# Kernel optimization log

Measured on AMD Instinct MI355X. Metric: run time of the kernel, lower is better.

Reference implementation:

```python
import jax, jax.numpy as jnp
import numpy as np

B, S, DIM = 8, 2048, 2048
M, N, DCTX = 4, 64, 1024
H, DH = 8, 64
INNER = H * DH
EPS = 1e-5


def _layernorm(x, g, b):
    mu = jnp.mean(x, axis=-1, keepdims=True)
    var = jnp.mean(jnp.square(x - mu), axis=-1, keepdims=True)
    return (x - mu) * jax.lax.rsqrt(var + EPS) * g + b


def setup_inputs() -> dict:
    key = jax.random.key(0)
    ks = jax.random.split(key, 5)
    return {
        "x": jax.random.normal(ks[0], (B, S, DIM), jnp.float32),
        "context": jax.random.normal(ks[1], (B, M, N, DCTX), jnp.float32),
        "ln_g": jnp.ones((DIM,), jnp.float32),
        "ln_b": jnp.zeros((DIM,), jnp.float32),
        "lnc_g": jnp.ones((DCTX,), jnp.float32),
        "lnc_b": jnp.zeros((DCTX,), jnp.float32),
        "Wq": jax.random.normal(ks[2], (DIM, INNER), jnp.float32) * (DIM ** -0.5),
        "Wkv": jax.random.normal(ks[3], (DCTX, 2 * INNER), jnp.float32) * (DCTX ** -0.5),
        "Wout": jax.random.normal(ks[4], (INNER, DIM), jnp.float32) * (INNER ** -0.5),
        "top_k": 32,
    }


def reference(x, context, ln_g, ln_b, lnc_g, lnc_b, Wq, Wkv, Wout, top_k):
    b, s, _ = x.shape
    kv_len = context.shape[1] * context.shape[2]
    scale = DH ** -0.5

    xn = _layernorm(x, ln_g, ln_b)                                  # [b, s, dim]
    cn = _layernorm(context.reshape(b, kv_len, DCTX), lnc_g, lnc_b)  # [b, mn, dctx]

    q = (xn @ Wq).reshape(b, s, H, DH).transpose(0, 2, 1, 3)        # [b, h, s, dh]
    kv = cn @ Wkv                                                   # [b, mn, 2*inner]
    k, v = jnp.split(kv, 2, axis=-1)
    k = k.reshape(b, kv_len, H, DH).transpose(0, 2, 1, 3)           # [b, h, mn, dh]
    v = v.reshape(b, kv_len, H, DH).transpose(0, 2, 1, 3)

    sim = jnp.einsum('bhid,bhjd->bhij', q, k) * scale               # [b, h, s, mn]
    topk_vals, topk_idx = jax.lax.top_k(sim, top_k)                 # [b, h, s, k]
    # softmax over -inf-masked sim == softmax over the top-k values scattered back
    attn_k = jax.nn.softmax(topk_vals, axis=-1)
    bi = jnp.arange(b)[:, None, None, None]
    hi = jnp.arange(H)[None, :, None, None]
    ii = jnp.arange(s)[None, None, :, None]
    attn = jnp.zeros_like(sim).at[bi, hi, ii, topk_idx].set(attn_k)  # [b, h, s, mn]

    out = jnp.einsum('bhij,bhjd->bhid', attn, v)                    # [b, h, s, dh]
    out = out.transpose(0, 2, 1, 3).reshape(b, s, INNER)
    return out @ Wout                                               # [b, s, dim]
```

## Files before the change

### kernel.cpp

```cpp
#include <hip/hip_runtime.h>
#include <hip/hip_bf16.h>


typedef __attribute__((ext_vector_type(8))) short short8;
typedef __attribute__((ext_vector_type(8))) _Float16 half8;
typedef __attribute__((ext_vector_type(4))) float f32x4;
typedef unsigned int u32;
typedef unsigned short u16;
typedef unsigned long long u64;

#define DI __device__ __forceinline__
#define DELTA 1.5e-4f
#define BLEND_GAP 5e-5
#define FCAP 131072u

DI u16 f2bf(float f) {
  u32 u = __builtin_bit_cast(u32, f);
  u = (u + 0x7FFFu + ((u >> 16) & 1u)) >> 16;
  return (u16)u;
}
DI float bf2f(u16 h) { u32 u = ((u32)h) << 16; return __builtin_bit_cast(float, u); }
DI u16 f2h(float f) { _Float16 h = (_Float16)f; return __builtin_bit_cast(u16, h); }
DI float h2f(u16 b) { return (float)__builtin_bit_cast(_Float16, b); }

DI f32x4 mfma16(short8 a, short8 b, f32x4 c) {
  return __builtin_amdgcn_mfma_f32_16x16x32_bf16(a, b, c, 0, 0, 0);
}
DI f32x4 mfma16h(half8 a, half8 b, f32x4 c) {
  return __builtin_amdgcn_mfma_f32_16x16x32_f16(a, b, c, 0, 0, 0);
}

DI void gload_lds16(const u16* g, u16* l) {
  __builtin_amdgcn_global_load_lds(
      (const __attribute__((address_space(1))) void*)g,
      (__attribute__((address_space(3))) void*)l, 16, 0, 0);
}

__global__ void k_zero(u32* p) { if (threadIdx.x < 8) p[threadIdx.x] = 0; }

__global__ __launch_bounds__(1024) void k_transpose_split(
    const float* __restrict__ src, u16* __restrict__ dh, u16* __restrict__ dl,
    int R, int C, float scale) {
  __shared__ float tile[32][33];
  const int tx = threadIdx.x, ty = threadIdx.y;
  const int c0 = blockIdx.x * 32, r0 = blockIdx.y * 32;
  tile[ty][tx] = src[(size_t)(r0 + ty) * C + (c0 + tx)];
  __syncthreads();
  const float f = tile[tx][ty] * scale;
  const u16 h = f2bf(f);
  const size_t o = (size_t)(c0 + ty) * R + (r0 + tx);
  dh[o] = h;
  dl[o] = f2bf(f - bf2f(h));
}

__global__ __launch_bounds__(1024) void k_transpose_f16(
    const float* __restrict__ src, u16* __restrict__ dst, int R, int C) {
  __shared__ float tile[32][33];
  const int tx = threadIdx.x, ty = threadIdx.y;
  const int c0 = blockIdx.x * 32, r0 = blockIdx.y * 32;
  tile[ty][tx] = src[(size_t)(r0 + ty) * C + (c0 + tx)];
  __syncthreads();
  dst[(size_t)(c0 + ty) * R + (r0 + tx)] = f2h(tile[tx][ty]);
}

__global__ __launch_bounds__(1024) void k_transpose_f32(
    const float* __restrict__ src, float* __restrict__ dst, int R, int C) {
  __shared__ float tile[32][33];
  const int tx = threadIdx.x, ty = threadIdx.y;
  const int c0 = blockIdx.x * 32, r0 = blockIdx.y * 32;
  tile[ty][tx] = src[(size_t)(r0 + ty) * C + (c0 + tx)];
  __syncthreads();
  dst[(size_t)(c0 + ty) * R + (r0 + tx)] = tile[tx][ty];
}

template<int C>
__global__ __launch_bounds__(256) void k_layernorm_split(
    const float* __restrict__ x, const float* __restrict__ g, const float* __restrict__ bb,
    u16* __restrict__ oh, u16* __restrict__ ol) {
  constexpr int NV = C / 256;
  const int t = threadIdx.x;
  const size_t row = blockIdx.x;
  const float* xr = x + row * C + t * NV;
  float v[NV]; float s = 0.f, sq = 0.f;
#pragma unroll
  for (int j = 0; j < NV; j += 4) {
    const float4 f = *(const float4*)(xr + j);
    v[j] = f.x; v[j + 1] = f.y; v[j + 2] = f.z; v[j + 3] = f.w;
    s += (f.x + f.y) + (f.z + f.w);
    sq += (f.x * f.x + f.y * f.y) + (f.z * f.z + f.w * f.w);
  }
#pragma unroll
  for (int off = 32; off >= 1; off >>= 1) { s += __shfl_xor(s, off); sq += __shfl_xor(sq, off); }
  __shared__ float red[8];
  if ((t & 63) == 0) { red[t >> 6] = s; red[4 + (t >> 6)] = sq; }
  __syncthreads();
  s = (red[0] + red[1]) + (red[2] + red[3]);
  sq = (red[4] + red[5]) + (red[6] + red[7]);
  const float mu = s * (1.0f / C);
  const float rs = rsqrtf(sq * (1.0f / C) - mu * mu + 1e-5f);
  u16 hh[NV], ll[NV];
#pragma unroll
  for (int j = 0; j < NV; j += 4) {
    const float4 gg = *(const float4*)(g + t * NV + j);
    const float4 bv = *(const float4*)(bb + t * NV + j);
    float f0 = (v[j] - mu) * rs * gg.x + bv.x;
    float f1 = (v[j + 1] - mu) * rs * gg.y + bv.y;
    float f2 = (v[j + 2] - mu) * rs * gg.z + bv.z;
    float f3 = (v[j + 3] - mu) * rs * gg.w + bv.w;
    hh[j] = f2bf(f0); ll[j] = f2bf(f0 - bf2f(hh[j]));
    hh[j + 1] = f2bf(f1); ll[j + 1] = f2bf(f1 - bf2f(hh[j + 1]));
    hh[j + 2] = f2bf(f2); ll[j + 2] = f2bf(f2 - bf2f(hh[j + 2]));
    hh[j + 3] = f2bf(f3); ll[j + 3] = f2bf(f3 - bf2f(hh[j + 3]));
  }
  if constexpr (NV == 8) {
    *(uint4*)(oh + row * C + t * NV) = *(const uint4*)hh;
    *(uint4*)(ol + row * C + t * NV) = *(const uint4*)ll;
  } else {
    *(uint2*)(oh + row * C + t * NV) = *(const uint2*)hh;
    *(uint2*)(ol + row * C + t * NV) = *(const uint2*)ll;
  }
}

__global__ __launch_bounds__(256) void k_gemm_split(
    const u16* __restrict__ Ah, const u16* __restrict__ Al,
    const u16* __restrict__ Bh, const u16* __restrict__ Bl,
    u16* __restrict__ Oh, u16* __restrict__ Ol, u16* __restrict__ Op,
    int M, int N, int K, int splitc) {
  __shared__ __align__(1024) u16 sAh[4096], sAl[4096], sBh[4096], sBl[4096];
  const int t = threadIdx.x;
  const int w = t >> 6, l = t & 63, lg = l >> 4, lr = l & 15;
  const int nwg = gridDim.x;
  const int cpx = nwg >> 3;
  const int swz = (blockIdx.x & 7) * cpx + (blockIdx.x >> 3);
  const int nbx = N >> 7;
  const size_t row0 = (size_t)(swz / nbx) * 128;
  const size_t col0 = (size_t)(swz % nbx) * 128;
  const size_t wrow0 = row0 + (size_t)(w >> 1) * 64;
  const size_t wcol0 = col0 + (size_t)(w & 1) * 64;
  const int srow0 = w * 32 + (l >> 2);
  const int skk = (l & 3) * 8;
  f32x4 acc[4][4];
  const f32x4 z4 = {0.f, 0.f, 0.f, 0.f};
#pragma unroll
  for (int i = 0; i < 4; ++i)
#pragma unroll
    for (int j = 0; j < 4; ++j) acc[i][j] = z4;
  for (int k0 = 0; k0 < K; k0 += 32) {
#pragma unroll
    for (int iss = 0; iss < 2; ++iss) {
      const int sr = srow0 + iss * 16;
      const int ub = (w * 32 + iss * 16) * 32;
      const size_t ga = (row0 + sr) * (size_t)K + k0 + skk;
      const size_t gb = (col0 + sr) * (size_t)K + k0 + skk;
      gload_lds16(Ah + ga, sAh + ub);
      gload_lds16(Al + ga, sAl + ub);
      gload_lds16(Bh + gb, sBh + ub);
      gload_lds16(Bl + gb, sBl + ub);
    }
    __syncthreads();
    short8 ah[4], al[4], bh[4], bl[4];
#pragma unroll
    for (int mt = 0; mt < 4; ++mt) {
      const int r = (w >> 1) * 64 + mt * 16 + lr;
      ah[mt] = *(const short8*)(sAh + r * 32 + lg * 8);
      al[mt] = *(const short8*)(sAl + r * 32 + lg * 8);
    }
#pragma unroll
    for (int nt = 0; nt < 4; ++nt) {
      const int c = (w & 1) * 64 + nt * 16 + lr;
      bh[nt] = *(const short8*)(sBh + c * 32 + lg * 8);
      bl[nt] = *(const short8*)(sBl + c * 32 + lg * 8);
    }
#pragma unroll
    for (int mt = 0; mt < 4; ++mt)
#pragma unroll
      for (int nt = 0; nt < 4; ++nt) {
        f32x4 a = acc[mt][nt];
        a = mfma16(al[mt], bh[nt], a);
        a = mfma16(ah[mt], bl[nt], a);
        a = mfma16(ah[mt], bh[nt], a);
        acc[mt][nt] = a;
      }
    __syncthreads();
  }
#pragma unroll
  for (int mt = 0; mt < 4; ++mt)
#pragma unroll
    for (int nt = 0; nt < 4; ++nt)
#pragma unroll
      for (int i = 0; i < 4; ++i) {
        const size_t r = wrow0 + mt * 16 + lg * 4 + i;
        const size_t c = wcol0 + nt * 16 + lr;
        const float f = acc[mt][nt][i];
        if ((int)c < splitc) {
          const u16 h = f2bf(f);
          Oh[r * (size_t)splitc + c] = h;
          Ol[r * (size_t)splitc + c] = f2bf(f - bf2f(h));
        } else {
          Op[r * (size_t)(N - splitc) + (c - splitc)] = f2h(f);
        }
      }
}

__global__ __launch_bounds__(256) void k_gemm_f16_f32(
    const u16* __restrict__ A, const u16* __restrict__ Bt, float* __restrict__ C,
    int M, int N, int K) {
  __shared__ __align__(1024) u16 sA[4096], sB[4096];
  const int t = threadIdx.x;
  const int w = t >> 6, l = t & 63, lg = l >> 4, lr = l & 15;
  const int nwg = gridDim.x;
  const int cpx = nwg >> 3;
  const int swz = (blockIdx.x & 7) * cpx + (blockIdx.x >> 3);
  const int nbx = N >> 7;
  const size_t row0 = (size_t)(swz / nbx) * 128;
  const size_t col0 = (size_t)(swz % nbx) * 128;
  const size_t wrow0 = row0 + (size_t)(w >> 1) * 64;
  const size_t wcol0 = col0 + (size_t)(w & 1) * 64;
  const int srow0 = w * 32 + (l >> 2);
  const int skk = (l & 3) * 8;
  f32x4 acc[4][4];
  const f32x4 z4 = {0.f, 0.f, 0.f, 0.f};
#pragma unroll
  for (int i = 0; i < 4; ++i)
#pragma unroll
    for (int j = 0; j < 4; ++j) acc[i][j] = z4;
  for (int k0 = 0; k0 < K; k0 += 32) {
#pragma unroll
    for (int iss = 0; iss < 2; ++iss) {
      const int sr = srow0 + iss * 16;
      const int ub = (w * 32 + iss * 16) * 32;
      const size_t ga = (row0 + sr) * (size_t)K + k0 + skk;
      const size_t gb = (col0 + sr) * (size_t)K + k0 + skk;
      gload_lds16(A + ga, sA + ub);
      gload_lds16(Bt + gb, sB + ub);
    }
    __syncthreads();
    half8 a[4], b[4];
#pragma unroll
    for (int mt = 0; mt < 4; ++mt) {
      const int r = (w >> 1) * 64 + mt * 16 + lr;
      a[mt] = __builtin_bit_cast(half8, *(const short8*)(sA + r * 32 + lg * 8));
    }
#pragma unroll
    for (int nt = 0; nt < 4; ++nt) {
      const int c = (w & 1) * 64 + nt * 16 + lr;
      b[nt] = __builtin_bit_cast(half8, *(const short8*)(sB + c * 32 + lg * 8));
    }
#pragma unroll
    for (int mt = 0; mt < 4; ++mt)
#pragma unroll
      for (int nt = 0; nt < 4; ++nt) acc[mt][nt] = mfma16h(a[mt], b[nt], acc[mt][nt]);
    __syncthreads();
  }
#pragma unroll
  for (int mt = 0; mt < 4; ++mt)
#pragma unroll
    for (int nt = 0; nt < 4; ++nt)
#pragma unroll
      for (int i = 0; i < 4; ++i)
        C[(wrow0 + mt * 16 + lg * 4 + i) * (size_t)N + wcol0 + nt * 16 + lr] = acc[mt][nt][i];
}

__global__ __launch_bounds__(256) void k_attn(
    const u16* __restrict__ qh, const u16* __restrict__ ql,
    const u16* __restrict__ kh, const u16* __restrict__ kl,
    const u16* __restrict__ vv, u16* __restrict__ ao,
    u32* __restrict__ fcnt, u32* __restrict__ flist) {
  extern __shared__ unsigned char smem[];
  unsigned char* khmem = smem;
  unsigned char* vmem = smem + 32768;

  const int t = threadIdx.x;
  const int gid = blockIdx.x;
  const int sblk = gid & 31, hh = (gid >> 5) & 7, b = gid >> 8;
  const size_t base = ((size_t)b * 256) * 512 + hh * 64;

  {
    const int jb = t >> 3;
    const int d0 = (t & 7) * 8;
#pragma unroll
    for (int rep = 0; rep < 8; ++rep) {
      const int j = rep * 32 + jb;
      const int sw = (j & 7) << 4;
      const uint4 kh4 = *(const uint4*)(kh + base + (size_t)j * 512 + d0);
      *(uint4*)(khmem + ((j * 128 + d0 * 2) ^ sw)) = kh4;
      const uint4 v4 = *(const uint4*)(vv + base + (size_t)j * 512 + d0);
      const u16* ev = (const u16*)&v4;
#pragma unroll
      for (int i = 0; i < 8; ++i) {
        const int d = d0 + i;
        const int mix = ((d & 7) ^ (d >> 3)) & 7;
        *(u16*)(vmem + ((d * 512 + j * 2) ^ (mix << 4))) = ev[i];
      }
    }
  }
  __syncthreads();

  const int w = t >> 6, l = t & 63, lg = l >> 4, lr = l & 15;
  const int s0 = sblk * 64 + w * 16;
  const u16* qpb = qh + ((size_t)(b * 2048 + s0 + lr)) * 512 + hh * 64 + lg * 8;
  const u16* qpl = ql + ((size_t)(b * 2048 + s0 + lr)) * 512 + hh * 64 + lg * 8;
  const short8 qh0 = *(const short8*)(qpb);
  const short8 qh1 = *(const short8*)(qpb + 32);
  const short8 ql0 = *(const short8*)(qpl);
  const short8 ql1 = *(const short8*)(qpl + 32);

  f32x4 acc[16];
  const f32x4 z4 = {0.f, 0.f, 0.f, 0.f};
#pragma unroll
  for (int ct = 0; ct < 16; ++ct) {
    const int j = ct * 16 + lr;
    const int sw = (j & 7) << 4;
    const short8 kB0 = *(const short8*)(khmem + ((j * 128 + lg * 16) ^ sw));
    const short8 kB1 = *(const short8*)(khmem + ((j * 128 + 64 + lg * 16) ^ sw));
    const short8 kC0 = *(const short8*)(kl + base + (size_t)j * 512 + lg * 8);
    const short8 kC1 = *(const short8*)(kl + base + (size_t)j * 512 + 32 + lg * 8);
    f32x4 z = z4;
    z = mfma16(ql0, kC0, z); z = mfma16(ql1, kC1, z);
    z = mfma16(ql0, kB0, z); z = mfma16(ql1, kB1, z);
    z = mfma16(qh0, kC0, z); z = mfma16(qh1, kC1, z);
    z = mfma16(qh0, kB0, z); z = mfma16(qh1, kB1, z);
    acc[ct] = z;
  }
  __syncthreads();

  unsigned char* wmem = khmem + w * 8192;
#pragma unroll
  for (int r = 0; r < 4; ++r) {
    float v[16]; u32 o[16];
#pragma unroll
    for (int c2 = 0; c2 < 16; ++c2) {
      const float f = acc[c2][r];
      v[c2] = f;
      const u32 u = __builtin_bit_cast(u32, f);
      o[c2] = (u & 0x80000000u) ? ~u : (u | 0x80000000u);
    }
    u32 lo = 0;
    for (int bit = 31; bit >= 0; --bit) {
      const u32 mid = lo | (1u << bit);
      int c = 0;
#pragma unroll
      for (int c2 = 0; c2 < 16; ++c2) c += (o[c2] >= mid) ? 1 : 0;
      c += __shfl_xor(c, 1); c += __shfl_xor(c, 2); c += __shfl_xor(c, 4); c += __shfl_xor(c, 8);
      lo = (c >= 32) ? mid : lo;
    }
    const u32 thr = lo;
    int cgt = 0; u32 m16 = 0;
#pragma unroll
    for (int c2 = 0; c2 < 16; ++c2) {
      cgt += (o[c2] > thr) ? 1 : 0;
      m16 |= (o[c2] == thr) ? (1u << c2) : 0u;
    }
    cgt += __shfl_xor(cgt, 1); cgt += __shfl_xor(cgt, 2); cgt += __shfl_xor(cgt, 4); cgt += __shfl_xor(cgt, 8);
    const int need = 32 - cgt;
    u32 selm = 0; int pre = 0;
#pragma unroll
    for (int c2 = 0; c2 < 16; ++c2) {
      const u64 bal = __ballot((int)((m16 >> c2) & 1u));
      const u32 gb = (u32)((bal >> (lg * 16)) & 0xFFFFull);
      const int rank = pre + __popc(gb & ((1u << lr) - 1u));
      selm |= (((m16 >> c2) & 1u) && rank < need) ? (1u << c2) : 0u;
      pre += __popc(gb);
    }
    {
      const u32 tu = (thr & 0x80000000u) ? (thr & 0x7FFFFFFFu) : ~thr;
      const float t32f = __builtin_bit_cast(float, tu);
      float m33 = -3.0e38f;
#pragma unroll
      for (int c2 = 0; c2 < 16; ++c2) {
        const bool se = (o[c2] > thr) || ((selm >> c2) & 1u);
        if (!se) m33 = fmaxf(m33, v[c2]);
      }
      m33 = fmaxf(m33, __shfl_xor(m33, 1)); m33 = fmaxf(m33, __shfl_xor(m33, 2));
      m33 = fmaxf(m33, __shfl_xor(m33, 4)); m33 = fmaxf(m33, __shfl_xor(m33, 8));
      if (lr == 0 && (t32f - m33) < DELTA) {
        const u32 pos = atomicAdd(fcnt, 1u);
        if (pos < FCAP)
          flist[pos] = (u32)((b << 14) | (hh << 11) | (s0 + lg * 4 + r));
      }
    }
    float mx = v[0];
#pragma unroll
    for (int c2 = 1; c2 < 16; ++c2) mx = fmaxf(mx, v[c2]);
    mx = fmaxf(mx, __shfl_xor(mx, 1)); mx = fmaxf(mx, __shfl_xor(mx, 2));
    mx = fmaxf(mx, __shfl_xor(mx, 4)); mx = fmaxf(mx, __shfl_xor(mx, 8));
    float wei[16]; float ws = 0.f;
#pragma unroll
    for (int c2 = 0; c2 < 16; ++c2) {
      const bool se = (o[c2] > thr) || ((selm >> c2) & 1u);
      const float e = se ? __expf(v[c2] - mx) : 0.f;
      wei[c2] = e; ws += e;
    }
    ws += __shfl_xor(ws, 1); ws += __shfl_xor(ws, 2); ws += __shfl_xor(ws, 4); ws += __shfl_xor(ws, 8);
    const float inv = 1.0f / ws;
    const int rowl = lg * 4 + r;
    const int swr = (rowl & 7) << 4;
#pragma unroll
    for (int c2 = 0; c2 < 16; ++c2)
      *(u16*)(wmem + ((rowl * 512 + (c2 * 16 + lr) * 2) ^ swr)) = f2h(wei[c2] * inv);
  }

  f32x4 oacc[4];
#pragma unroll
  for (int i = 0; i < 4; ++i) oacc[i] = z4;
#pragma unroll
  for (int ks = 0; ks < 8; ++ks) {
    const int k0 = ks * 32;
    const half8 aw = __builtin_bit_cast(half8,
        *(const short8*)(wmem + ((lr * 512 + (k0 + lg * 8) * 2) ^ ((lr & 7) << 4))));
#pragma unroll
    for (int ct = 0; ct < 4; ++ct) {
      const int d = ct * 16 + lr;
      const int mix = ((d & 7) ^ (d >> 3)) & 7;
      const half8 bv = __builtin_bit_cast(half8,
          *(const short8*)(vmem + ((d * 512 + (k0 + lg * 8) * 2) ^ (mix << 4))));
      oacc[ct] = mfma16h(aw, bv, oacc[ct]);
    }
  }
  u16* ob = ao + ((size_t)(b * 2048 + s0)) * 512 + hh * 64;
#pragma unroll
  for (int ct = 0; ct < 4; ++ct)
#pragma unroll
    for (int i = 0; i < 4; ++i)
      ob[(size_t)(lg * 4 + i) * 512 + ct * 16 + lr] = f2h(oacc[ct][i]);
}

__global__ __launch_bounds__(256) void k_ln_f64(
    const float* __restrict__ ctx, const float* __restrict__ g, const float* __restrict__ bb,
    double* __restrict__ out) {
  const size_t row = blockIdx.x;
  const float* xr = ctx + row * 1024;
  const int t = threadIdx.x;
  double sm = 0, sq = 0;
  float v[4];
#pragma unroll
  for (int j = 0; j < 4; ++j) { v[j] = xr[t * 4 + j]; sm += (double)v[j]; sq += (double)v[j] * (double)v[j]; }
  for (int o = 32; o >= 1; o >>= 1) { sm += __shfl_xor(sm, o); sq += __shfl_xor(sq, o); }
  __shared__ double red[16];
  if ((t & 63) == 0) { red[t >> 6] = sm; red[8 + (t >> 6)] = sq; }
  __syncthreads();
  sm = red[0] + red[1] + red[2] + red[3];
  sq = red[8] + red[9] + red[10] + red[11];
  const double mu = sm / 1024.0;
  const double rs = 1.0 / sqrt(sq / 1024.0 - mu * mu + 1e-5);
#pragma unroll
  for (int j = 0; j < 4; ++j)
    out[row * 1024 + t * 4 + j] = ((double)v[j] - mu) * rs * (double)g[t * 4 + j] + (double)bb[t * 4 + j];
}

__global__ __launch_bounds__(256) void k_gemm_f64(
    const double* __restrict__ A, const float* __restrict__ Wkv, double* __restrict__ K64) {
  __shared__ double As[64][33];
  __shared__ double Bs[32][65];
  const int t = threadIdx.x;
  const int ty = t >> 4, tx = t & 15;
  const int r0 = blockIdx.y * 64, c0 = blockIdx.x * 64;
  double acc[4][4] = {};
  for (int kk = 0; kk < 1024; kk += 32) {
#pragma unroll
    for (int i = 0; i < 8; ++i) {
      const int e = t + i * 256;
      const int r = e >> 5, k = e & 31;
      As[r][k] = A[(size_t)(r0 + r) * 1024 + kk + k];
    }
#pragma unroll
    for (int i = 0; i < 8; ++i) {
      const int e = t + i * 256;
      const int k = e >> 6, c = e & 63;
      Bs[k][c] = (double)Wkv[(size_t)(kk + k) * 1024 + c0 + c];
    }
    __syncthreads();
#pragma unroll 8
    for (int k3 = 0; k3 < 32; ++k3) {
      double av[4], bv[4];
#pragma unroll
      for (int i = 0; i < 4; ++i) av[i] = As[ty * 4 + i][k3];
#pragma unroll
      for (int j = 0; j < 4; ++j) bv[j] = Bs[k3][tx * 4 + j];
#pragma unroll
      for (int i = 0; i < 4; ++i)
#pragma unroll
        for (int j = 0; j < 4; ++j) acc[i][j] += av[i] * bv[j];
    }
    __syncthreads();
  }
#pragma unroll
  for (int i = 0; i < 4; ++i)
#pragma unroll
    for (int j = 0; j < 4; ++j)
      K64[(size_t)(r0 + ty * 4 + i) * 512 + c0 + tx * 4 + j] = acc[i][j];
}

__global__ __launch_bounds__(256) void k_cleanup(
    const float* __restrict__ x, const float* __restrict__ g, const float* __restrict__ bb,
    const float* __restrict__ wqT32, const double* __restrict__ k64,
    const u16* __restrict__ vf, u16* __restrict__ ao,
    const u32* __restrict__ fcnt, const u32* __restrict__ flist) {
  __shared__ double xn_s[2048];
  __shared__ double q_s[64];
  __shared__ double qp_s[4][64];
  __shared__ double sim_s[256];
  __shared__ double w_s[256];
  __shared__ double red_s[256];
  __shared__ double g32_s, g33_s;
  const int t = threadIdx.x;
  const u32 nf = fcnt[0];
  const u32 n = nf < FCAP ? nf : FCAP;
  for (u32 idx = blockIdx.x; idx < n; idx += gridDim.x) {
    const u32 rid = flist[idx];
    const int b = rid >> 14, h = (rid >> 11) & 7, s = rid & 2047;
    const float* xr = x + ((size_t)(b * 2048 + s)) * 2048;
    double sm = 0, sq = 0;
    for (int k = t; k < 2048; k += 256) { const double v = xr[k]; sm += v; sq += v * v; }
    for (int o = 32; o >= 1; o >>= 1) { sm += __shfl_xor(sm, o); sq += __shfl_xor(sq, o); }
    if ((t & 63) == 0) { red_s[t >> 6] = sm; red_s[8 + (t >> 6)] = sq; }
    __syncthreads();
    sm = red_s[0] + red_s[1] + red_s[2] + red_s[3];
    sq = red_s[8] + red_s[9] + red_s[10] + red_s[11];
    const double mu = sm / 2048.0;
    const double rs = 1.0 / sqrt(sq / 2048.0 - mu * mu + 1e-5);
    __syncthreads();
    for (int k = t; k < 2048; k += 256)
      xn_s[k] = ((double)xr[k] - mu) * rs * (double)g[k] + (double)bb[k];
    __syncthreads();
    const int d = t & 63, part = t >> 6;
    {
      const float* wrow = wqT32 + (size_t)(h * 64 + d) * 2048 + part * 512;
      const double* xp = xn_s + part * 512;
      double p0 = 0, p1 = 0, p2 = 0, p3 = 0;
#pragma unroll 4
      for (int k = 0; k < 512; k += 4) {
        const float4 wv = *(const float4*)(wrow + k);
        p0 += xp[k] * (double)wv.x;
        p1 += xp[k + 1] * (double)wv.y;
        p2 += xp[k + 2] * (double)wv.z;
        p3 += xp[k + 3] * (double)wv.w;
      }
      qp_s[part][d] = (p0 + p1) + (p2 + p3);
    }
    __syncthreads();
    if (t < 64) q_s[t] = qp_s[0][t] + qp_s[1][t] + qp_s[2][t] + qp_s[3][t];
    __syncthreads();
    const double* krow = k64 + ((size_t)(b * 256 + t)) * 512 + h * 64;
    double sim = 0;
#pragma unroll 8
    for (int dd = 0; dd < 64; ++dd) sim += q_s[dd] * krow[dd];
    sim_s[t] = sim * 0.125;
    __syncthreads();
    const double my = sim_s[t];
    int c = 0;
#pragma unroll 8
    for (int i = 0; i < 256; ++i) {
      const double si = sim_s[i];
      c += (si > my || (si == my && i < t)) ? 1 : 0;
    }
    const bool sel = c < 32;
    if (c == 31) g32_s = my;
    if (c == 32) g33_s = my;
    __syncthreads();
    const bool blend = (g32_s - g33_s) < BLEND_GAP;
    __syncthreads();
    red_s[t] = sel ? my : -1e300;
    __syncthreads();
    for (int o2 = 128; o2 >= 1; o2 >>= 1) {
      if (t < o2) red_s[t] = fmax(red_s[t], red_s[t + o2]);
      __syncthreads();
    }
    const double m = red_s[0];
    __syncthreads();
    double e = sel ? exp(my - m) : 0.0;
    if (blend && (c == 31 || c == 32)) e = 0.5 * exp(my - m);
    red_s[t] = e;
    __syncthreads();
    for (int o2 = 128; o2 >= 1; o2 >>= 1) {
      if (t < o2) red_s[t] += red_s[t + o2];
      __syncthreads();
    }
    const double Z = red_s[0];
    w_s[t] = e / Z;
    __syncthreads();
    if (t < 64) {
      double acc = 0;
      const u16* vcol = vf + ((size_t)(b * 256)) * 512 + h * 64 + t;
      for (int j = 0; j < 256; ++j) acc += w_s[j] * (double)h2f(vcol[(size_t)j * 512]);
      ao[((size_t)(b * 2048 + s)) * 512 + h * 64 + t] = f2h((float)acc);
    }
    __syncthreads();
  }
}

extern "C" void kernel_launch(void* const* d_in, const int* in_sizes, int n_in,
                              void* d_out, int out_size, void* d_ws, size_t ws_size,
                              hipStream_t stream) {
  (void)in_sizes; (void)n_in; (void)out_size; (void)ws_size;
  const float* x     = (const float*)d_in[0];
  const float* ctx   = (const float*)d_in[1];
  const float* ln_g  = (const float*)d_in[2];
  const float* ln_b  = (const float*)d_in[3];
  const float* lnc_g = (const float*)d_in[4];
  const float* lnc_b = (const float*)d_in[5];
  const float* Wq    = (const float*)d_in[6];
  const float* Wkv   = (const float*)d_in[7];
  const float* Wout  = (const float*)d_in[8];

  char* ws = (char*)d_ws;
  const size_t MB = 1048576;
  u16*   xn_h  = (u16*)(ws + 0);
  u16*   xn_l  = (u16*)(ws + 64 * MB);
  u16*   cn_h  = (u16*)(ws + 128 * MB);
  u16*   cn_l  = (u16*)(ws + 132 * MB);
  u16*   wqT_h = (u16*)(ws + 136 * MB);
  u16*   wqT_l = (u16*)(ws + 138 * MB);
  u16*   wkT_h = (u16*)(ws + 140 * MB);
  u16*   wkT_l = (u16*)(ws + 142 * MB);
  u16*   woT16 = (u16*)(ws + 144 * MB);
  float* wqT32 = (float*)(ws + 146 * MB);
  u16*   q_h   = (u16*)(ws + 150 * MB);
  u16*   q_l   = (u16*)(ws + 166 * MB);
  u16*   k_h   = (u16*)(ws + 182 * MB);
  u16*   k_l   = (u16*)(ws + 184 * MB);
  u16*   v_16  = (u16*)(ws + 186 * MB);
  u16*   ao16  = (u16*)(ws + 188 * MB);
  u32*   fcnt  = (u32*)(ws + 204 * MB);
  u32*   flist = (u32*)(ws + 204 * MB + 128);
  double* cn64 = (double*)(ws + 0);
  double* k64  = (double*)(ws + 16 * MB);

  const dim3 tb(32, 32);
  k_zero<<<1, 64, 0, stream>>>(fcnt);
  k_transpose_split<<<dim3(512 / 32, 2048 / 32), tb, 0, stream>>>(Wq, wqT_h, wqT_l, 2048, 512, 0.125f);
  k_transpose_split<<<dim3(1024 / 32, 1024 / 32), tb, 0, stream>>>(Wkv, wkT_h, wkT_l, 1024, 1024, 1.0f);
  k_transpose_f16<<<dim3(2048 / 32, 512 / 32), tb, 0, stream>>>(Wout, woT16, 512, 2048);
  k_transpose_f32<<<dim3(512 / 32, 2048 / 32), tb, 0, stream>>>(Wq, wqT32, 2048, 512);

  k_layernorm_split<2048><<<16384, 256, 0, stream>>>(x, ln_g, ln_b, xn_h, xn_l);
  k_layernorm_split<1024><<<2048, 256, 0, stream>>>(ctx, lnc_g, lnc_b, cn_h, cn_l);

  k_gemm_split<<<512, 256, 0, stream>>>(
      xn_h, xn_l, wqT_h, wqT_l, q_h, q_l, q_h, 16384, 512, 2048, 512);
  k_gemm_split<<<128, 256, 0, stream>>>(
      cn_h, cn_l, wkT_h, wkT_l, k_h, k_l, v_16, 2048, 1024, 1024, 512);

  k_ln_f64<<<2048, 256, 0, stream>>>(ctx, lnc_g, lnc_b, cn64);
  k_gemm_f64<<<dim3(8, 32), 256, 0, stream>>>(cn64, Wkv, k64);

  k_attn<<<2048, 256, 65536, stream>>>(q_h, q_l, k_h, k_l, v_16, ao16, fcnt, flist);

  k_cleanup<<<2048, 256, 0, stream>>>(x, ln_g, ln_b, wqT32, k64, v_16, ao16, fcnt, flist);

  k_gemm_f16_f32<<<2048, 256, 0, stream>>>(
      ao16, woT16, (float*)d_out, 16384, 2048, 512);
}
```

Baseline: 815.5 us.

## Pre-transpose V globally and read it from memory in attention instead of LDS

A new u16 transpose kernel writes V once as a [inner, b*mn] array before attention. The attention kernel no longer stages V into shared memory with scattered 2-byte transposed stores; its PV MFMA loop reads 16-byte V fragments straight from the pre-transposed global buffer. This halves the dynamic shared memory per block, which should let more blocks fit per CU. In exchange it adds an extra kernel launch and makes the PV loop depend on global/L2 latency, with strided row accesses.

```diff
diff --git a/kernel.cpp b/kernel.cpp
--- a/kernel.cpp
+++ b/kernel.cpp
@@ -66,6 +66,16 @@
 __global__ __launch_bounds__(1024) void k_transpose_f32(
     const float* __restrict__ src, float* __restrict__ dst, int R, int C) {
   __shared__ float tile[32][33];
+  const int tx = threadIdx.x, ty = threadIdx.y;
+  const int c0 = blockIdx.x * 32, r0 = blockIdx.y * 32;
+  tile[ty][tx] = src[(size_t)(r0 + ty) * C + (c0 + tx)];
+  __syncthreads();
+  dst[(size_t)(c0 + ty) * R + (r0 + tx)] = tile[tx][ty];
+}
+
+__global__ __launch_bounds__(1024) void k_transpose_u16(
+    const u16* __restrict__ src, u16* __restrict__ dst, int R, int C) {
+  __shared__ u16 tile[32][33];
   const int tx = threadIdx.x, ty = threadIdx.y;
   const int c0 = blockIdx.x * 32, r0 = blockIdx.y * 32;
   tile[ty][tx] = src[(size_t)(r0 + ty) * C + (c0 + tx)];
@@ -264,11 +274,10 @@
 __global__ __launch_bounds__(256) void k_attn(
     const u16* __restrict__ qh, const u16* __restrict__ ql,
     const u16* __restrict__ kh, const u16* __restrict__ kl,
-    const u16* __restrict__ vv, u16* __restrict__ ao,
+    const u16* __restrict__ vT, u16* __restrict__ ao,
     u32* __restrict__ fcnt, u32* __restrict__ flist) {
   extern __shared__ unsigned char smem[];
   unsigned char* khmem = smem;
-  unsigned char* vmem = smem + 32768;
 
   const int t = threadIdx.x;
   const int gid = blockIdx.x;
@@ -282,16 +291,8 @@
     for (int rep = 0; rep < 8; ++rep) {
       const int j = rep * 32 + jb;
       const int sw = (j & 7) << 4;
-      const uint4 kh4 = *(const uint4*)(kh + base + (size_t)j * 512 + d0);
-      *(uint4*)(khmem + ((j * 128 + d0 * 2) ^ sw)) = kh4;
-      const uint4 v4 = *(const uint4*)(vv + base + (size_t)j * 512 + d0);
-      const u16* ev = (const u16*)&v4;
-#pragma unroll
-      for (int i = 0; i < 8; ++i) {
-        const int d = d0 + i;
-        const int mix = ((d & 7) ^ (d >> 3)) & 7;
-        *(u16*)(vmem + ((d * 512 + j * 2) ^ (mix << 4))) = ev[i];
-      }
+      *(uint4*)(khmem + ((j * 128 + d0 * 2) ^ sw)) =
+          *(const uint4*)(kh + base + (size_t)j * 512 + d0);
     }
   }
   __syncthreads();
@@ -400,6 +401,7 @@
       *(u16*)(wmem + ((rowl * 512 + (c2 * 16 + lr) * 2) ^ swr)) = f2h(wei[c2] * inv);
   }
 
+  const size_t vtb = (size_t)(hh * 64) * 2048 + b * 256;
   f32x4 oacc[4];
 #pragma unroll
   for (int i = 0; i < 4; ++i) oacc[i] = z4;
@@ -411,9 +413,8 @@
 #pragma unroll
     for (int ct = 0; ct < 4; ++ct) {
       const int d = ct * 16 + lr;
-      const int mix = ((d & 7) ^ (d >> 3)) & 7;
       const half8 bv = __builtin_bit_cast(half8,
-          *(const short8*)(vmem + ((d * 512 + (k0 + lg * 8) * 2) ^ (mix << 4))));
+          *(const short8*)(vT + vtb + (size_t)d * 2048 + k0 + lg * 8));
       oacc[ct] = mfma16h(aw, bv, oacc[ct]);
     }
   }
@@ -623,6 +624,7 @@
   u16*   ao16  = (u16*)(ws + 188 * MB);
   u32*   fcnt  = (u32*)(ws + 204 * MB);
   u32*   flist = (u32*)(ws + 204 * MB + 128);
+  u16*   vT16  = (u16*)(ws + 205 * MB);
   double* cn64 = (double*)(ws + 0);
   double* k64  = (double*)(ws + 16 * MB);
 
@@ -641,10 +643,12 @@
   k_gemm_split<<<128, 256, 0, stream>>>(
       cn_h, cn_l, wkT_h, wkT_l, k_h, k_l, v_16, 2048, 1024, 1024, 512);
 
+  k_transpose_u16<<<dim3(512 / 32, 2048 / 32), tb, 0, stream>>>(v_16, vT16, 2048, 512);
+
   k_ln_f64<<<2048, 256, 0, stream>>>(ctx, lnc_g, lnc_b, cn64);
   k_gemm_f64<<<dim3(8, 32), 256, 0, stream>>>(cn64, Wkv, k64);
 
-  k_attn<<<2048, 256, 65536, stream>>>(q_h, q_l, k_h, k_l, v_16, ao16, fcnt, flist);
+  k_attn<<<2048, 256, 32768, stream>>>(q_h, q_l, k_h, k_l, vT16, ao16, fcnt, flist);
 
   k_cleanup<<<2048, 256, 0, stream>>>(x, ln_g, ln_b, wqT32, k64, v_16, ao16, fcnt, flist);
 
```

Result: faster. 786.5 us (-3.6%).
